# Kernel tuning notes

Measured on AMD Instinct MI355X. Metric: run time of the kernel, lower is better.

## Reference

```python
import jax, jax.numpy as jnp
import numpy as np

# Config matching init_kwargs: 63 single-grapheme tokens + optional blank -> C = 64,
# trivial (identity) lexicon, ngram = 0 (no transition model), allow_repeats = True.
# Under this config the GTN composition (target chain o lexicon -> tokens graph ->
# alignments, intersected with linear emission graph, forward_score) is exactly the
# CTC forward algorithm over the extended label sequence z = [blank, y1, blank, ...,
# yL, blank], with the s-2 -> s skip allowed for ALL non-blank states (allow_repeats).

B, T, C, L = 128, 3000, 64, 128
NEG = -1e30  # effective -inf, safe in fp32


def setup_inputs() -> dict:
    key = jax.random.key(0)
    k1, k2 = jax.random.split(key)
    inputs = jax.random.normal(k1, (B, T, C), dtype=jnp.float32)  # raw logits
    # target token ids in [0, C-2]; blank = C-1 is never a target
    targets = jax.random.randint(k2, (B, L), 0, C - 1, dtype=jnp.int32)
    return {"inputs": inputs, "targets": targets}


def reference(inputs, targets):
    Bv, Tv, Cv = inputs.shape
    Lv = targets.shape[1]
    S = 2 * Lv + 1
    blank = Cv - 1
    # transitions is None -> module applies log_softmax to inputs
    logp = jax.nn.log_softmax(inputs, axis=2)  # [B, T, C]
    # extended label sequence: blanks at even positions, targets at odd positions
    z = jnp.full((Bv, S), blank, dtype=jnp.int32).at[:, 1::2].set(targets)  # [B, S]
    # per-frame emission scores for each extended state: [B, T, S] -> [T, B, S]
    em = jnp.take_along_axis(logp, jnp.broadcast_to(z[:, None, :], (Bv, Tv, S)), axis=2)
    em = jnp.transpose(em, (1, 0, 2))
    # skip transition (s-2 -> s) allowed for every non-blank (odd) state because
    # allow_repeats=True (no z[s] != z[s-2] restriction)
    skip_ok = (jnp.arange(S) % 2 == 1)  # [S]

    alpha0 = (jnp.full((Bv, S), NEG, dtype=jnp.float32)
              .at[:, 0].set(em[0, :, 0])
              .at[:, 1].set(em[0, :, 1]))

    def step(alpha, e_t):
        a1 = jnp.pad(alpha[:, :-1], ((0, 0), (1, 0)), constant_values=NEG)
        a2 = jnp.pad(alpha[:, :-2], ((0, 0), (2, 0)), constant_values=NEG)
        a2 = jnp.where(skip_ok[None, :], a2, NEG)
        new = e_t + jax.scipy.special.logsumexp(jnp.stack([alpha, a1, a2], axis=0), axis=0)
        return new, None

    alphaT, _ = jax.lax.scan(step, alpha0, em[1:])  # [B, S]
    # accepting states: last label (S-2) and trailing blank (S-1)
    ll = jax.scipy.special.logsumexp(alphaT[:, S - 2:S], axis=1)  # [B]
    # reduction='none' -> scales = 1; forward returns torch.mean over batch
    return jnp.mean(-ll)
```

## Files before the change

kernel.cpp:

```cpp
#include <hip/hip_runtime.h>
#include <stdint.h>

#define BB 128
#define TT 3000
#define CC 64
#define LL 128
#define NEGf (-1e30f)
#define LOG2E 1.4426950408889634f
#define LN2f 0.6931471805599453f
#define F 12
#define NCH 250
#define NBUF 5
#define NPH (NCH + 3)
#define LSE_BLOCKS 512

typedef float f32x2 __attribute__((ext_vector_type(2)));
typedef float f32x4 __attribute__((ext_vector_type(4)));

__device__ __forceinline__ float fexp2(float x){ return __builtin_amdgcn_exp2f(x); }
__device__ __forceinline__ float flog2(float x){ return __builtin_amdgcn_logf(x); }
__device__ __forceinline__ float shr1_neg(float x){
    int r = __builtin_amdgcn_update_dpp(__float_as_int(NEGf), __float_as_int(x),
                                        0x138, 0xF, 0xF, false);
    return __int_as_float(r);
}
#define DPPMAXT(x,c) fmaxf((x),__int_as_float(__builtin_amdgcn_update_dpp(0,__float_as_int(x),(c),0xF,0xF,true)))
#define DPPADDT(x,c) ((x)+__int_as_float(__builtin_amdgcn_update_dpp(0,__float_as_int(x),(c),0xF,0xF,true)))
#define RED64(OP,x) { x=OP(x,0x111); x=OP(x,0x112); x=OP(x,0x114); x=OP(x,0x118); x=OP(x,0x142); x=OP(x,0x143); }

__global__ __launch_bounds__(512) void fused_kernel(const float* __restrict__ in,
                                                    const int* __restrict__ tgt,
                                                    float* __restrict__ lse,
                                                    float* __restrict__ ll2){
    __shared__ float emR[NBUF][F][132];
    __shared__ __align__(16) float bndR[4][3][F];
    __shared__ float laL[3008];
    __shared__ float lbL[3008];
    if (blockIdx.x < BB) {
        const int b = blockIdx.x;
        const int wave = threadIdx.x >> 6;
        const int lane = threadIdx.x & 63;
        const float* fb = in + (size_t)b * TT * CC;
        const uint32_t em_base  = (uint32_t)(uintptr_t)&emR[0][0][0];
        const uint32_t bnd_base = (uint32_t)(uintptr_t)&bndR[0][0][0];

        if (wave < 4) {
            const int w = wave;
            __builtin_amdgcn_s_setprio(1);
            if (w == 0) {
                if (lane < 36) (&bndR[0][0][0])[lane] = NEGf;
                if (lane >= 1 && lane <= 3) bndR[lane][0][0] = NEGf;
                if (lane < 8) { laL[3000+lane] = NEGf; lbL[3000+lane] = 0.f; }
            }
            const bool odd = (lane & 1);
            const uint32_t em_off = odd ? (uint32_t)(32*w + (lane>>1))*4u : 512u;
            float aa = (w==0 && lane==0) ? 0.f : NEGf;
            __syncthreads();
            for (int ph = 0; ph < NPH; ++ph) {
                const int x = ph - w;
                if (x >= 0 && x < NCH) {
                    const uint32_t buf = (uint32_t)(x % NBUF);
                    const uint32_t ra  = em_base + buf*(F*132u*4u) + em_off;
                    const uint32_t xm3 = (uint32_t)(x % 3);
                    const uint32_t xp3 = (uint32_t)((x+1) % 3);
                    const uint32_t rb  = bnd_base + (uint32_t)w*144u + xm3*48u;
                    f32x4 B4a, B4b, B4c; float ef[F]; float hist[F];
                    asm volatile("ds_read_b128 %0, %1 offset:0"  : "=v"(B4a) : "v"(rb));
                    asm volatile("ds_read_b128 %0, %1 offset:16" : "=v"(B4b) : "v"(rb));
                    asm volatile("ds_read_b128 %0, %1 offset:32" : "=v"(B4c) : "v"(rb));
                    asm volatile("ds_read_b32 %0, %1 offset:0"    : "=v"(ef[0]) : "v"(ra));
                    asm volatile("ds_read_b32 %0, %1 offset:528"  : "=v"(ef[1]) : "v"(ra));
                    asm volatile("ds_read_b32 %0, %1 offset:1056" : "=v"(ef[2]) : "v"(ra));
                    #pragma unroll
                    for (int j = 0; j < F; ++j) {
                        if (j + 3 < F)
                            asm volatile("ds_read_b32 %0, %1 offset:%2"
                                         : "=v"(ef[j+3]) : "v"(ra), "n"((j+3)*528));
                        if (j < F-3)       asm volatile("s_waitcnt lgkmcnt(3)" ::: "memory");
                        else if (j == F-3) asm volatile("s_waitcnt lgkmcnt(2)" ::: "memory");
                        else if (j == F-2) asm volatile("s_waitcnt lgkmcnt(1)" ::: "memory");
                        else               asm volatile("s_waitcnt lgkmcnt(0)" ::: "memory");
                        __builtin_amdgcn_sched_barrier(0);
                        float bj = (j < 4) ? B4a[j & 3] : ((j < 8) ? B4b[j & 3] : B4c[j & 3]);
                        float p1 = shr1_neg(aa);
                        float p2 = shr1_neg(p1);
                        p1 = (lane==0) ? bj : p1;
                        p2 = (lane==1) ? bj : p2;
                        float z = odd ? p2 : NEGf;
                        float mx = fmaxf(fmaxf(aa,p1),z);
                        float md = __builtin_amdgcn_fmed3f(aa,p1,z);
                        float mn = fminf(fminf(aa,p1),z);
                        float e  = fexp2(md-mx) + fexp2(mn-mx);
                        float v  = __builtin_fmaf(e,0.5f,-0.5f);
                        float h  = __builtin_fmaf(v,0.2f,-0.25f);
                        h = __builtin_fmaf(v,h,0.33333333f);
                        h = __builtin_fmaf(v,h,-0.5f);
                        h = __builtin_fmaf(v,h,1.0f);
                        aa = __builtin_fmaf(v*h, LOG2E, mx+1.0f) + ef[j];
                        hist[j] = aa;
                    }
                    if (w < 3 && lane == 63) {
                        float* reg = &bndR[w+1][0][0];
                        #pragma unroll
                        for (int j = 0; j < F-1; ++j) reg[xm3*F + j + 1] = hist[j];
                        reg[xp3*F + 0] = hist[F-1];
                    }
                    if (w == 3 && lane == 63) {
                        #pragma unroll
                        for (int j = 0; j < F; ++j) laL[x*F + j] = hist[j];
                    }
                    asm volatile("s_waitcnt lgkmcnt(0)" ::: "memory");
                }
                __syncthreads();
            }
            __syncthreads();
            if (w == 0) {
                const int base = lane*47;
                float seg = 0.f;
                for (int k = 0; k < 47; ++k) seg += lbL[base+k];
                float inc = seg;
                #pragma unroll
                for (int d = 1; d < 64; d <<= 1) {
                    float t = __shfl_up(inc, d, 64);
                    if (lane >= d) inc += t;
                }
                float CBtot = __int_as_float(__builtin_amdgcn_readlane(__float_as_int(inc), 63));
                float ex = inc - seg;
                float cb = ex, gm = NEGf;
                for (int k = 0; k < 47; ++k) {
                    int idx = base+k;
                    cb += lbL[idx];
                    float g = laL[idx] + (CBtot - cb);
                    g = (idx == 2999) ? NEGf : g;
                    gm = fmaxf(gm, g);
                }
                RED64(DPPMAXT, gm);
                float gmax = __int_as_float(__builtin_amdgcn_readlane(__float_as_int(gm), 63));
                cb = ex; float se = 0.f;
                for (int k = 0; k < 47; ++k) {
                    int idx = base+k;
                    cb += lbL[idx];
                    float g = laL[idx] + (CBtot - cb);
                    g = (idx == 2999) ? NEGf : g;
                    se += fexp2(g - gmax);
                }
                RED64(DPPADDT, se);
                float S = __int_as_float(__builtin_amdgcn_readlane(__float_as_int(se), 63));
                float la256 = gmax + flog2(S);
                float la255f = laL[2999];
                float m = fmaxf(la255f, la256);
                float r = m + flog2(1.0f + fexp2(-fabsf(la255f - la256)));
                if (lane == 0) ll2[b] = r;
            }
        } else {
            const int p = wave - 4;
            const int t0 = tgt[b*LL + 2*lane];
            const int t1 = tgt[b*LL + 2*lane + 1];
            float v0[3], v1[3], vb[3];
            auto loadc = [&](int cc) {
                const float* cbase = fb + (size_t)cc * F * CC;
                #pragma unroll
                for (int k = 0; k < 3; ++k) {
                    const float* fr = cbase + (3*p + k)*CC;
                    v0[k] = fr[t0]; v1[k] = fr[t1]; vb[k] = fr[63];
                }
            };
            auto storec = [&](int cc) {
                const int buf = cc % NBUF;
                #pragma unroll
                for (int k = 0; k < 3; ++k) {
                    const int f = 3*p + k;
                    f32x2 wv; wv.x = v0[k]*LOG2E; wv.y = v1[k]*LOG2E;
                    *(f32x2*)&emR[buf][f][2*lane] = wv;
                    if (lane == 0) {
                        float xb = vb[k]*LOG2E;
                        emR[buf][f][128] = xb;
                        lbL[cc*F + f] = xb;
                    }
                }
            };
            loadc(0); storec(0); loadc(1);
            __syncthreads();
            for (int ph = 0; ph < NPH; ++ph) {
                if (ph + 1 < NCH) storec(ph + 1);
                if (ph + 2 < NCH) loadc(ph + 2);
                __syncthreads();
            }
            __syncthreads();
        }
        return;
    }
    int wv = (blockIdx.x - BB) * 8 + (threadIdx.x >> 6);
    int lane = threadIdx.x & 63;
    const int stride = LSE_BLOCKS * 8;
    for (int row = wv; row < BB * TT; row += stride) {
        float x = in[(size_t)row * CC + lane];
        float m = x;
        #pragma unroll
        for (int d = 32; d >= 1; d >>= 1) m = fmaxf(m, __shfl_xor(m, d, 64));
        float s = fexp2((x - m) * LOG2E);
        #pragma unroll
        for (int d = 32; d >= 1; d >>= 1) s += __shfl_xor(s, d, 64);
        if (lane == 0) lse[row] = m + flog2(s) * LN2f;
    }
}

__global__ __launch_bounds__(256) void bsum_kernel(const float* __restrict__ lse,
                                                   const float* __restrict__ ll2,
                                                   float* __restrict__ lossb) {
    __shared__ float red[256];
    int b = blockIdx.x;
    float s = 0.f;
    for (int i = threadIdx.x; i < TT; i += 256) s += lse[(size_t)b * TT + i];
    red[threadIdx.x] = s;
    __syncthreads();
    #pragma unroll
    for (int w = 128; w >= 1; w >>= 1) {
        if (threadIdx.x < w) red[threadIdx.x] += red[threadIdx.x + w];
        __syncthreads();
    }
    if (threadIdx.x == 0) lossb[b] = red[0] - ll2[b] * LN2f;
}

__global__ __launch_bounds__(64) void final_kernel(const float* __restrict__ lossb,
                                                   float* __restrict__ out) {
    int lane = threadIdx.x;
    float v = lossb[lane] + lossb[lane + 64];
    #pragma unroll
    for (int d = 32; d >= 1; d >>= 1) v += __shfl_xor(v, d, 64);
    if (lane == 0) out[0] = v / (float)BB;
}

extern "C" void kernel_launch(void* const* d_in, const int* in_sizes, int n_in,
                              void* d_out, int out_size, void* d_ws, size_t ws_size,
                              hipStream_t stream) {
    const float* in = (const float*)d_in[0];
    const int* tg = (const int*)d_in[1];
    float* out = (float*)d_out;
    float* lse = (float*)d_ws;
    float* ll2 = lse + (size_t)BB * TT;
    float* lossb = ll2 + BB;

    hipLaunchKernelGGL(fused_kernel, dim3(BB + LSE_BLOCKS), dim3(512), 0, stream,
                       in, tg, lse, ll2);
    hipLaunchKernelGGL(bsum_kernel, dim3(BB), dim3(256), 0, stream, lse, ll2, lossb);
    hipLaunchKernelGGL(final_kernel, dim3(1), dim3(64), 0, stream, lossb, out);
}
```

Baseline: 264.2 us.

## Switch CTC recurrence to linear-domain mantissa/exponent pairs with two-state-per-lane waves

Replaces the log-domain logsumexp recurrence (exp2 plus polynomial log) with a split representation of an integer exponent plus a normalized mantissa, so each step uses ldexp, adds and bit manipulation instead of transcendental-heavy work. Each lane now holds both the blank and label state for one target, which halves the compute waves from four to two and shortens the wavefront pipeline. Producers precompute emissions as exponent/mantissa pairs in shared memory with three buffers. This risks precision and range handling differences and adds more LDS traffic per step.

After: 280.7 us. +6.2%, slower.

```diff
diff --git a/kernel.cpp b/kernel.cpp
--- a/kernel.cpp
+++ b/kernel.cpp
@@ -10,8 +10,8 @@
 #define LN2f 0.6931471805599453f
 #define F 12
 #define NCH 250
-#define NBUF 5
-#define NPH (NCH + 3)
+#define NPH (NCH + 1)
+#define NULLM (-30000)
 #define LSE_BLOCKS 512
 
 typedef float f32x2 __attribute__((ext_vector_type(2)));
@@ -19,8 +19,11 @@
 
 __device__ __forceinline__ float fexp2(float x){ return __builtin_amdgcn_exp2f(x); }
 __device__ __forceinline__ float flog2(float x){ return __builtin_amdgcn_logf(x); }
-__device__ __forceinline__ float shr1_neg(float x){
-    int r = __builtin_amdgcn_update_dpp(__float_as_int(NEGf), __float_as_int(x),
+__device__ __forceinline__ int dpp_shr1_i(int x, int old){
+    return __builtin_amdgcn_update_dpp(old, x, 0x138, 0xF, 0xF, false);
+}
+__device__ __forceinline__ float dpp_shr1_f(float x, float old){
+    int r = __builtin_amdgcn_update_dpp(__float_as_int(old), __float_as_int(x),
                                         0x138, 0xF, 0xF, false);
     return __int_as_float(r);
 }
@@ -32,8 +35,9 @@
                                                     const int* __restrict__ tgt,
                                                     float* __restrict__ lse,
                                                     float* __restrict__ ll2){
-    __shared__ float emR[NBUF][F][132];
-    __shared__ __align__(16) float bndR[4][3][F];
+    __shared__ __align__(16) float emR[3][F][258];
+    __shared__ __align__(16) float bndR[3][F][2];
+    __shared__ __align__(16) float nullBnd[24];
     __shared__ float laL[3008];
     __shared__ float lbL[3008];
     if (blockIdx.x < BB) {
@@ -44,77 +48,99 @@
         const uint32_t em_base  = (uint32_t)(uintptr_t)&emR[0][0][0];
         const uint32_t bnd_base = (uint32_t)(uintptr_t)&bndR[0][0][0];
 
-        if (wave < 4) {
-            const int w = wave;
+        if (wave < 2) {
+            const int W = wave;
             __builtin_amdgcn_s_setprio(1);
-            if (w == 0) {
-                if (lane < 36) (&bndR[0][0][0])[lane] = NEGf;
-                if (lane >= 1 && lane <= 3) bndR[lane][0][0] = NEGf;
+            if (W == 0) {
+                if (lane < 12) { nullBnd[2*lane] = __int_as_float(NULLM); nullBnd[2*lane+1] = 0.5f; }
+                if (lane == 0) { bndR[0][0][0] = __int_as_float(NULLM); bndR[0][0][1] = 0.5f; }
                 if (lane < 8) { laL[3000+lane] = NEGf; lbL[3000+lane] = 0.f; }
             }
-            const bool odd = (lane & 1);
-            const uint32_t em_off = odd ? (uint32_t)(32*w + (lane>>1))*4u : 512u;
-            float aa = (w==0 && lane==0) ? 0.f : NEGf;
+            int a0m = NULLM, a1m = NULLM; float a0r = 0.5f, a1r = 0.5f;
+            if (W == 0 && lane == 0) { a0m = 1; a0r = 0.5f; }
+            const uint32_t em1_ad = em_base + (uint32_t)((64*W + lane) * 8);
+            const uint32_t emB_ad = em_base + 1024u;
+            const uint32_t nb_ad  = (uint32_t)(uintptr_t)&nullBnd[0];
             __syncthreads();
             for (int ph = 0; ph < NPH; ++ph) {
-                const int x = ph - w;
+                const int x = ph - W;
                 if (x >= 0 && x < NCH) {
-                    const uint32_t buf = (uint32_t)(x % NBUF);
-                    const uint32_t ra  = em_base + buf*(F*132u*4u) + em_off;
-                    const uint32_t xm3 = (uint32_t)(x % 3);
-                    const uint32_t xp3 = (uint32_t)((x+1) % 3);
-                    const uint32_t rb  = bnd_base + (uint32_t)w*144u + xm3*48u;
-                    f32x4 B4a, B4b, B4c; float ef[F]; float hist[F];
-                    asm volatile("ds_read_b128 %0, %1 offset:0"  : "=v"(B4a) : "v"(rb));
-                    asm volatile("ds_read_b128 %0, %1 offset:16" : "=v"(B4b) : "v"(rb));
-                    asm volatile("ds_read_b128 %0, %1 offset:32" : "=v"(B4c) : "v"(rb));
-                    asm volatile("ds_read_b32 %0, %1 offset:0"    : "=v"(ef[0]) : "v"(ra));
-                    asm volatile("ds_read_b32 %0, %1 offset:528"  : "=v"(ef[1]) : "v"(ra));
-                    asm volatile("ds_read_b32 %0, %1 offset:1056" : "=v"(ef[2]) : "v"(ra));
+                    const uint32_t buf = (uint32_t)(x % 3);
+                    const uint32_t ra = em1_ad + buf*12384u;
+                    const uint32_t rb = emB_ad + buf*12384u;
+                    const uint32_t rq = W ? (bnd_base + buf*96u) : nb_ad;
+                    f32x4 B4[6]; f32x2 E1[F], EB[F];
+                    asm volatile("ds_read_b128 %0, %1 offset:0"  : "=v"(B4[0]) : "v"(rq));
+                    asm volatile("ds_read_b128 %0, %1 offset:16" : "=v"(B4[1]) : "v"(rq));
+                    asm volatile("ds_read_b128 %0, %1 offset:32" : "=v"(B4[2]) : "v"(rq));
+                    asm volatile("ds_read_b128 %0, %1 offset:48" : "=v"(B4[3]) : "v"(rq));
+                    asm volatile("ds_read_b128 %0, %1 offset:64" : "=v"(B4[4]) : "v"(rq));
+                    asm volatile("ds_read_b128 %0, %1 offset:80" : "=v"(B4[5]) : "v"(rq));
+                    asm volatile("ds_read_b64 %0, %1 offset:0"    : "=v"(E1[0]) : "v"(ra));
+                    asm volatile("ds_read_b64 %0, %1 offset:0"    : "=v"(EB[0]) : "v"(rb));
+                    asm volatile("ds_read_b64 %0, %1 offset:1032" : "=v"(E1[1]) : "v"(ra));
+                    asm volatile("ds_read_b64 %0, %1 offset:1032" : "=v"(EB[1]) : "v"(rb));
+                    asm volatile("ds_read_b64 %0, %1 offset:2064" : "=v"(E1[2]) : "v"(ra));
+                    asm volatile("ds_read_b64 %0, %1 offset:2064" : "=v"(EB[2]) : "v"(rb));
+                    int hm[F]; float hr[F];
                     #pragma unroll
                     for (int j = 0; j < F; ++j) {
-                        if (j + 3 < F)
-                            asm volatile("ds_read_b32 %0, %1 offset:%2"
-                                         : "=v"(ef[j+3]) : "v"(ra), "n"((j+3)*528));
-                        if (j < F-3)       asm volatile("s_waitcnt lgkmcnt(3)" ::: "memory");
-                        else if (j == F-3) asm volatile("s_waitcnt lgkmcnt(2)" ::: "memory");
-                        else if (j == F-2) asm volatile("s_waitcnt lgkmcnt(1)" ::: "memory");
-                        else               asm volatile("s_waitcnt lgkmcnt(0)" ::: "memory");
+                        if (j + 3 < F) {
+                            asm volatile("ds_read_b64 %0, %1 offset:%2"
+                                         : "=v"(E1[j+3]) : "v"(ra), "n"((j+3)*1032));
+                            asm volatile("ds_read_b64 %0, %1 offset:%2"
+                                         : "=v"(EB[j+3]) : "v"(rb), "n"((j+3)*1032));
+                            asm volatile("s_waitcnt lgkmcnt(6)" ::: "memory");
+                        } else if (j + 3 == F) {
+                            asm volatile("s_waitcnt lgkmcnt(4)" ::: "memory");
+                        } else if (j + 2 == F) {
+                            asm volatile("s_waitcnt lgkmcnt(2)" ::: "memory");
+                        } else {
+                            asm volatile("s_waitcnt lgkmcnt(0)" ::: "memory");
+                        }
                         __builtin_amdgcn_sched_barrier(0);
-                        float bj = (j < 4) ? B4a[j & 3] : ((j < 8) ? B4b[j & 3] : B4c[j & 3]);
-                        float p1 = shr1_neg(aa);
-                        float p2 = shr1_neg(p1);
-                        p1 = (lane==0) ? bj : p1;
-                        p2 = (lane==1) ? bj : p2;
-                        float z = odd ? p2 : NEGf;
-                        float mx = fmaxf(fmaxf(aa,p1),z);
-                        float md = __builtin_amdgcn_fmed3f(aa,p1,z);
-                        float mn = fminf(fminf(aa,p1),z);
-                        float e  = fexp2(md-mx) + fexp2(mn-mx);
-                        float v  = __builtin_fmaf(e,0.5f,-0.5f);
-                        float h  = __builtin_fmaf(v,0.2f,-0.25f);
-                        h = __builtin_fmaf(v,h,0.33333333f);
-                        h = __builtin_fmaf(v,h,-0.5f);
-                        h = __builtin_fmaf(v,h,1.0f);
-                        aa = __builtin_fmaf(v*h, LOG2E, mx+1.0f) + ef[j];
-                        hist[j] = aa;
-                    }
-                    if (w < 3 && lane == 63) {
-                        float* reg = &bndR[w+1][0][0];
+                        const int   bjm = __float_as_int((j&1) ? B4[j>>1].z : B4[j>>1].x);
+                        const float bjr = (j&1) ? B4[j>>1].w : B4[j>>1].y;
+                        const int   e1m = __float_as_int(E1[j].x); const float e1r = E1[j].y;
+                        const int   ebm = __float_as_int(EB[j].x); const float ebr = EB[j].y;
+                        int p1m = dpp_shr1_i(a1m, NULLM);
+                        float p1r = dpp_shr1_f(a1r, 0.5f);
+                        p1m = (lane == 0) ? bjm : p1m;
+                        p1r = (lane == 0) ? bjr : p1r;
+                        int Mt = (a0m > p1m) ? a0m : p1m;
+                        float rs = ldexpf(a0r, a0m - Mt) + ldexpf(p1r, p1m - Mt);
+                        int ui = __float_as_int(rs);
+                        int n0m = Mt + ((ui >> 23) - 126) + ebm;
+                        float n0r = __int_as_float((ui & 0x7FFFFF) | 0x3F000000) * ebr;
+                        int Mu = (a1m > a0m) ? a1m : a0m; Mu = (Mu > p1m) ? Mu : p1m;
+                        float ru = ldexpf(a1r, a1m - Mu) + ldexpf(a0r, a0m - Mu)
+                                 + ldexpf(p1r, p1m - Mu);
+                        int uj = __float_as_int(ru);
+                        int n1m = Mu + ((uj >> 23) - 126) + e1m;
+                        float n1r = __int_as_float((uj & 0x7FFFFF) | 0x3F000000) * e1r;
+                        a0m = n0m; a0r = n0r; a1m = n1m; a1r = n1r;
+                        hm[j] = a1m; hr[j] = a1r;
+                    }
+                    if (W == 0 && lane == 63) {
+                        float* s0 = &bndR[x % 3][0][0];
                         #pragma unroll
-                        for (int j = 0; j < F-1; ++j) reg[xm3*F + j + 1] = hist[j];
-                        reg[xp3*F + 0] = hist[F-1];
-                    }
-                    if (w == 3 && lane == 63) {
+                        for (int j = 0; j < F-1; ++j) {
+                            s0[(j+1)*2] = __int_as_float(hm[j]); s0[(j+1)*2+1] = hr[j];
+                        }
+                        float* s1 = &bndR[(x+1) % 3][0][0];
+                        s1[0] = __int_as_float(hm[F-1]); s1[1] = hr[F-1];
+                    }
+                    if (W == 1 && lane == 63) {
                         #pragma unroll
-                        for (int j = 0; j < F; ++j) laL[x*F + j] = hist[j];
+                        for (int j = 0; j < F; ++j)
+                            laL[x*F + j] = (float)hm[j] + flog2(hr[j]);
                     }
                     asm volatile("s_waitcnt lgkmcnt(0)" ::: "memory");
                 }
                 __syncthreads();
             }
             __syncthreads();
-            if (w == 0) {
+            if (W == 0) {
                 const int base = lane*47;
                 float seg = 0.f;
                 for (int k = 0; k < 47; ++k) seg += lbL[base+k];
@@ -153,28 +179,33 @@
                 if (lane == 0) ll2[b] = r;
             }
         } else {
-            const int p = wave - 4;
-            const int t0 = tgt[b*LL + 2*lane];
-            const int t1 = tgt[b*LL + 2*lane + 1];
-            float v0[3], v1[3], vb[3];
-            auto loadc = [&](int cc) {
+            const int p = wave - 2;
+            const int t0 = tgt[b*LL + lane];
+            const int t1 = tgt[b*LL + 64 + lane];
+            float v0[2], v1[2], vb[2];
+            auto loadc = [&](int cc){
                 const float* cbase = fb + (size_t)cc * F * CC;
                 #pragma unroll
-                for (int k = 0; k < 3; ++k) {
-                    const float* fr = cbase + (3*p + k)*CC;
+                for (int k = 0; k < 2; ++k) {
+                    const float* fr = cbase + (p + 6*k) * CC;
                     v0[k] = fr[t0]; v1[k] = fr[t1]; vb[k] = fr[63];
                 }
             };
-            auto storec = [&](int cc) {
-                const int buf = cc % NBUF;
+            auto storec = [&](int cc){
+                const int buf = cc % 3;
                 #pragma unroll
-                for (int k = 0; k < 3; ++k) {
-                    const int f = 3*p + k;
-                    f32x2 wv; wv.x = v0[k]*LOG2E; wv.y = v1[k]*LOG2E;
-                    *(f32x2*)&emR[buf][f][2*lane] = wv;
+                for (int k = 0; k < 2; ++k) {
+                    const int f = p + 6*k;
+                    float x0 = v0[k] * LOG2E; float f0 = floorf(x0);
+                    *(f32x2*)&emR[buf][f][2*lane] =
+                        (f32x2){__int_as_float((int)f0 + 1), fexp2(x0 - f0 - 1.0f)};
+                    float x1 = v1[k] * LOG2E; float f1 = floorf(x1);
+                    *(f32x2*)&emR[buf][f][2*(64+lane)] =
+                        (f32x2){__int_as_float((int)f1 + 1), fexp2(x1 - f1 - 1.0f)};
                     if (lane == 0) {
-                        float xb = vb[k]*LOG2E;
-                        emR[buf][f][128] = xb;
+                        float xb = vb[k] * LOG2E; float fbl = floorf(xb);
+                        *(f32x2*)&emR[buf][f][256] =
+                            (f32x2){__int_as_float((int)fbl + 1), fexp2(xb - fbl - 1.0f)};
                         lbL[cc*F + f] = xb;
                     }
                 }
```
